# Kernel optimization log

Hardware: AMD Instinct MI355X
Metric: run time of the kernel (lower is better)

Reference implementation:

```python
import jax, jax.numpy as jnp
import numpy as np

B, S, D = 8, 1024, 768
H, DH = 8, 96          # number_of_heads, head_outdim = D // H
DFF = 4 * D            # mlp hidden
EPS = 1e-5


def _p(key, shape, scale=0.02):
    return (jax.random.normal(key, shape, dtype=jnp.float32) * scale)


def setup_inputs() -> dict:
    key = jax.random.key(0)
    ks = jax.random.split(key, 16)
    return {
        "h": jax.random.normal(ks[0], (B, S, D), dtype=jnp.float32),
        "x": jax.random.normal(ks[1], (B, S, D), dtype=jnp.float32),
        # SLN 1: scalar gamma/beta + LayerNorm affine
        "g1": jnp.ones((), jnp.float32), "be1": jnp.zeros((), jnp.float32),
        "ln1_w": jnp.ones((D,), jnp.float32), "ln1_b": jnp.zeros((D,), jnp.float32),
        # SLN 2
        "g2": jnp.ones((), jnp.float32), "be2": jnp.zeros((), jnp.float32),
        "ln2_w": jnp.ones((D,), jnp.float32), "ln2_b": jnp.zeros((D,), jnp.float32),
        # MSA projections (stored as [in, out] for x @ W)
        "Wq": _p(ks[2], (D, H * DH)), "bq": jnp.zeros((H * DH,), jnp.float32),
        "Wk": _p(ks[3], (D, H * DH)), "bk": jnp.zeros((H * DH,), jnp.float32),
        "Wv": _p(ks[4], (D, H * DH)), "bv": jnp.zeros((H * DH,), jnp.float32),
        "Wo": _p(ks[5], (H * DH, D)), "bo": jnp.zeros((D,), jnp.float32),
        # MLP: D -> 4D -> D, relu
        "W1": _p(ks[6], (D, DFF)), "b1": jnp.zeros((DFF,), jnp.float32),
        "W2": _p(ks[7], (DFF, D)), "b2": jnp.zeros((D,), jnp.float32),
    }


def _sln(h, x, gamma, beta, w, b):
    # SLN(h, x) = gamma * x * LayerNorm(h) + beta * x
    mu = jnp.mean(h, axis=-1, keepdims=True)
    var = jnp.var(h, axis=-1, keepdims=True)
    ln = (h - mu) * jax.lax.rsqrt(var + EPS) * w + b
    return gamma * x * ln + beta * x


def _l2_msa(h, Wq, bq, Wk, bk, Wv, bv, Wo, bo):
    # L2-distance multi-head self-attention (lp=2)
    def heads(W, bias):
        y = h @ W + bias                      # [B,S,H*DH]
        return y.reshape(B, S, H, DH).transpose(0, 2, 1, 3)  # [B,H,S,DH]
    q, k, v = heads(Wq, bq), heads(Wk, bk), heads(Wv, bv)
    # pairwise L2 distances via the quadratic expansion (avoids [B,H,S,S,DH])
    q2 = jnp.sum(q * q, axis=-1)              # [B,H,S]
    k2 = jnp.sum(k * k, axis=-1)              # [B,H,S]
    qk = jnp.einsum("bhsd,bhtd->bhst", q, k)  # [B,H,S,S]
    d2 = jnp.maximum(q2[..., :, None] + k2[..., None, :] - 2.0 * qk, 0.0)
    dist = jnp.sqrt(d2)                       # cdist(q, k, p=2)
    attn = jax.nn.softmax(-dist / np.sqrt(DH), axis=-1)
    out = jnp.einsum("bhst,bhtd->bhsd", attn, v)  # [B,H,S,DH]
    out = out.transpose(0, 2, 1, 3).reshape(B, S, H * DH)
    return out @ Wo + bo


def reference(h, x, g1, be1, ln1_w, ln1_b, g2, be2, ln2_w, ln2_b,
              Wq, bq, Wk, bk, Wv, bv, Wo, bo, W1, b1, W2, b2):
    h1 = _sln(h, x, g1, be1, ln1_w, ln1_b)
    htmp = _l2_msa(h1, Wq, bq, Wk, bk, Wv, bv, Wo, bo) + h   # dropout_rate=0 -> identity
    h2 = _sln(htmp, x, g2, be2, ln2_w, ln2_b)
    hf = jax.nn.relu(h2 @ W1 + b1) @ W2 + b2 + htmp
    return (x, hf)
```

## Files before the change

kernel.cpp:

```cpp
#include <hip/hip_runtime.h>
#include <math.h>

#define B_ 8
#define S_ 1024
#define D_ 768
#define H_ 8
#define DH_ 96
#define DFF_ 3072
#define NTOK (B_*S_)
#define QKVW 2304
#define EPS_ 1e-5f

typedef __attribute__((ext_vector_type(4))) float f4;
typedef __attribute__((ext_vector_type(4))) int i4;
typedef __attribute__((ext_vector_type(8))) __bf16 bf16x8;
typedef __attribute__((ext_vector_type(4))) unsigned short us4;
typedef __attribute__((ext_vector_type(8))) unsigned short us8;

static __device__ __forceinline__ unsigned short f2bf(float f) {
    unsigned int u = __builtin_bit_cast(unsigned int, f);
    u += 0x7fffu + ((u >> 16) & 1u);
    return (unsigned short)(u >> 16);
}
static __device__ __forceinline__ float bf2f(unsigned short u) {
    unsigned int x = ((unsigned int)u) << 16;
    return __builtin_bit_cast(float, x);
}

#define GLOBAL_LOAD_LDS16(g, l) \
    __builtin_amdgcn_global_load_lds((const __attribute__((address_space(1))) unsigned int*)(g), \
                                     (__attribute__((address_space(3))) unsigned int*)(l), 16, 0, 0)

__global__ __launch_bounds__(192) void sln_kernel(
    const float* __restrict__ h, const float* __restrict__ x,
    const float* __restrict__ gamma, const float* __restrict__ beta,
    const float* __restrict__ w, const float* __restrict__ bvec,
    unsigned short* __restrict__ out_bf, float* __restrict__ xcopy)
{
    int row = blockIdx.x;
    int t = threadIdx.x;
    const float4* h4 = (const float4*)(h + (size_t)row * D_);
    const float4* x4 = (const float4*)(x + (size_t)row * D_);
    float4 hv = h4[t];
    float s  = hv.x + hv.y + hv.z + hv.w;
    float ss = hv.x*hv.x + hv.y*hv.y + hv.z*hv.z + hv.w*hv.w;
    #pragma unroll
    for (int off = 32; off > 0; off >>= 1) {
        s  += __shfl_down(s, off);
        ss += __shfl_down(ss, off);
    }
    __shared__ float red[2][3];
    int wid = t >> 6;
    if ((t & 63) == 0) { red[0][wid] = s; red[1][wid] = ss; }
    __syncthreads();
    float sum   = red[0][0] + red[0][1] + red[0][2];
    float sumsq = red[1][0] + red[1][1] + red[1][2];
    float mu  = sum * (1.0f / D_);
    float var = sumsq * (1.0f / D_) - mu * mu;
    float rstd = rsqrtf(var + EPS_);
    float g = gamma[0], be = beta[0];
    float4 wv = ((const float4*)w)[t];
    float4 bv = ((const float4*)bvec)[t];
    float4 xv = x4[t];
    us4 o;
    o.x = f2bf(xv.x * (g * ((hv.x - mu) * rstd * wv.x + bv.x) + be));
    o.y = f2bf(xv.y * (g * ((hv.y - mu) * rstd * wv.y + bv.y) + be));
    o.z = f2bf(xv.z * (g * ((hv.z - mu) * rstd * wv.z + bv.z) + be));
    o.w = f2bf(xv.w * (g * ((hv.w - mu) * rstd * wv.w + bv.w) + be));
    *(us4*)(out_bf + (size_t)row * D_ + t * 4) = o;
    if (xcopy) ((float4*)(xcopy + (size_t)row * D_))[t] = xv;
}

__global__ __launch_bounds__(256) void prep_all_kernel(
    const float* __restrict__ Wq, const float* __restrict__ Wk,
    const float* __restrict__ Wv, const float* __restrict__ Wo,
    const float* __restrict__ W1, const float* __restrict__ W2,
    const float* __restrict__ bq, const float* __restrict__ bk, const float* __restrict__ bv,
    unsigned short* __restrict__ Wqkvt, unsigned short* __restrict__ Wot,
    unsigned short* __restrict__ W1t, unsigned short* __restrict__ W2t,
    float* __restrict__ bqkv)
{
    int id = blockIdx.x;
    int tx = threadIdx.x, ty = threadIdx.y;
    if (id >= 6912) {
        int i = (id - 6912) * 256 + ty * 32 + tx;
        if (i < QKVW) {
            float v = (i < 768) ? bq[i] : (i < 1536) ? bk[i - 768] : bv[i - 1536];
            bqkv[i] = v;
        }
        return;
    }
    const float* in; unsigned short* out; int K, N, nbx, rel;
    if (id < 1728)      { int m = id / 576; rel = id % 576;
                          in = (m == 0) ? Wq : (m == 1) ? Wk : Wv;
                          out = Wqkvt + (size_t)m * 768 * 768; K = 768; N = 768; nbx = 24; }
    else if (id < 2304) { rel = id - 1728; in = Wo; out = Wot;  K = 768;  N = 768;  nbx = 24; }
    else if (id < 4608) { rel = id - 2304; in = W1; out = W1t;  K = 768;  N = 3072; nbx = 96; }
    else                { rel = id - 4608; in = W2; out = W2t;  K = 3072; N = 768;  nbx = 24; }
    int n0 = (rel % nbx) * 32, k0 = (rel / nbx) * 32;
    __shared__ float tile[32][33];
    #pragma unroll
    for (int r = 0; r < 4; r++)
        tile[ty + r * 8][tx] = in[(size_t)(k0 + ty + r * 8) * N + n0 + tx];
    __syncthreads();
    #pragma unroll
    for (int r = 0; r < 4; r++)
        out[(size_t)(n0 + ty + r * 8) * K + k0 + tx] = f2bf(tile[tx][ty + r * 8]);
}

template<int OUT_BF16, int RELU>
__global__ __launch_bounds__(256) void gemm_mfma_kernel(
    const unsigned short* __restrict__ A, const unsigned short* __restrict__ Bt,
    const float* __restrict__ bias, const float* __restrict__ resid,
    void* __restrict__ Cout, int M, int N, int K)
{
    __shared__ unsigned short Asm[2][128 * 32];
    __shared__ unsigned short Bsm[2][128 * 32];

    int t = threadIdx.x;
    int lane = t & 63, wv = t >> 6;
    int wm = wv & 1, wn = wv >> 1;
    int l16 = lane & 15, quad = lane >> 4;

    int bm = blockIdx.x * 128;
    int bn = blockIdx.y * 128;

    const unsigned short* Abase = A  + (size_t)bm * K;
    const unsigned short* Bbase = Bt + (size_t)bn * K;

    int fl0 = t, fl1 = 256 + t;
    int r0 = fl0 >> 2, lg0 = (fl0 ^ (fl0 >> 3)) & 3;
    int r1 = fl1 >> 2, lg1 = (fl1 ^ (fl1 >> 3)) & 3;

    f4 acc[4][4] = {};

    GLOBAL_LOAD_LDS16(Abase + (size_t)r0 * K + lg0 * 8, &Asm[0][fl0 * 8]);
    GLOBAL_LOAD_LDS16(Abase + (size_t)r1 * K + lg1 * 8, &Asm[0][fl1 * 8]);
    GLOBAL_LOAD_LDS16(Bbase + (size_t)r0 * K + lg0 * 8, &Bsm[0][fl0 * 8]);
    GLOBAL_LOAD_LDS16(Bbase + (size_t)r1 * K + lg1 * 8, &Bsm[0][fl1 * 8]);
    __syncthreads();

    int nk = K >> 5;
    int cur = 0;
    for (int it = 0; it < nk; ++it) {
        if (it + 1 < nk) {
            int k0 = (it + 1) << 5;
            GLOBAL_LOAD_LDS16(Abase + (size_t)r0 * K + k0 + lg0 * 8, &Asm[cur ^ 1][fl0 * 8]);
            GLOBAL_LOAD_LDS16(Abase + (size_t)r1 * K + k0 + lg1 * 8, &Asm[cur ^ 1][fl1 * 8]);
            GLOBAL_LOAD_LDS16(Bbase + (size_t)r0 * K + k0 + lg0 * 8, &Bsm[cur ^ 1][fl0 * 8]);
            GLOBAL_LOAD_LDS16(Bbase + (size_t)r1 * K + k0 + lg1 * 8, &Bsm[cur ^ 1][fl1 * 8]);
        }

        bf16x8 xf[4], wf[4];
        #pragma unroll
        for (int i = 0; i < 4; i++) {
            int m = wm * 64 + i * 16 + l16;
            int p = (quad ^ (m >> 1)) & 3;
            xf[i] = __builtin_bit_cast(bf16x8, *(const i4*)&Asm[cur][m * 32 + p * 8]);
        }
        #pragma unroll
        for (int j = 0; j < 4; j++) {
            int n = wn * 64 + j * 16 + l16;
            int p = (quad ^ (n >> 1)) & 3;
            wf[j] = __builtin_bit_cast(bf16x8, *(const i4*)&Bsm[cur][n * 32 + p * 8]);
        }
        #pragma unroll
        for (int j = 0; j < 4; j++)
            #pragma unroll
            for (int i = 0; i < 4; i++)
                acc[j][i] = __builtin_amdgcn_mfma_f32_16x16x32_bf16(wf[j], xf[i], acc[j][i], 0, 0, 0);

        __syncthreads();
        cur ^= 1;
    }

    #pragma unroll
    for (int i = 0; i < 4; i++) {
        int rowg = bm + wm * 64 + i * 16 + l16;
        #pragma unroll
        for (int j = 0; j < 4; j++) {
            int colg0 = bn + wn * 64 + j * 16 + quad * 4;
            f4 v = acc[j][i];
            f4 b4 = *(const f4*)&bias[colg0];
            v += b4;
            if (RELU) {
                #pragma unroll
                for (int r = 0; r < 4; r++) v[r] = fmaxf(v[r], 0.f);
            }
            if (resid) {
                f4 r4 = *(const f4*)&resid[(size_t)rowg * N + colg0];
                v += r4;
            }
            if (OUT_BF16) {
                us4 o;
                o.x = f2bf(v[0]); o.y = f2bf(v[1]); o.z = f2bf(v[2]); o.w = f2bf(v[3]);
                *(us4*)((unsigned short*)Cout + (size_t)rowg * N + colg0) = o;
            } else {
                *(f4*)((float*)Cout + (size_t)rowg * N + colg0) = v;
            }
        }
    }
}

template<int OUT_BF16, int RELU>
__global__ __launch_bounds__(256) void gemm_mfma_n64_kernel(
    const unsigned short* __restrict__ A, const unsigned short* __restrict__ Bt,
    const float* __restrict__ bias, const float* __restrict__ resid,
    void* __restrict__ Cout, int M, int N, int K)
{
    __shared__ unsigned short Asm[2][128 * 64];
    __shared__ unsigned short Bsm[2][64 * 64];

    int t = threadIdx.x;
    int lane = t & 63, wv = t >> 6;
    int wm = wv & 1, wn = wv >> 1;
    int l16 = lane & 15, quad = lane >> 4;

    int bm = blockIdx.x * 128;
    int bn = blockIdx.y * 64;

    const unsigned short* Abase = A  + (size_t)bm * K;
    const unsigned short* Bbase = Bt + (size_t)bn * K;

    int ar[4], alg[4], br[2], blg[2];
    #pragma unroll
    for (int i = 0; i < 4; i++) {
        int fl = t + i * 256;
        ar[i] = fl >> 3; alg[i] = (fl ^ (fl >> 3)) & 7;
    }
    #pragma unroll
    for (int i = 0; i < 2; i++) {
        int fl = t + i * 256;
        br[i] = fl >> 3; blg[i] = (fl ^ (fl >> 3)) & 7;
    }

    f4 acc[2][4] = {};

    #pragma unroll
    for (int i = 0; i < 4; i++)
        GLOBAL_LOAD_LDS16(Abase + (size_t)ar[i] * K + alg[i] * 8, &Asm[0][(t + i * 256) * 8]);
    #pragma unroll
    for (int i = 0; i < 2; i++)
        GLOBAL_LOAD_LDS16(Bbase + (size_t)br[i] * K + blg[i] * 8, &Bsm[0][(t + i * 256) * 8]);
    __syncthreads();

    int nk = K >> 6;
    int cur = 0;
    for (int it = 0; it < nk; ++it) {
        if (it + 1 < nk) {
            int k0 = (it + 1) << 6;
            #pragma unroll
            for (int i = 0; i < 4; i++)
                GLOBAL_LOAD_LDS16(Abase + (size_t)ar[i] * K + k0 + alg[i] * 8, &Asm[cur ^ 1][(t + i * 256) * 8]);
            #pragma unroll
            for (int i = 0; i < 2; i++)
                GLOBAL_LOAD_LDS16(Bbase + (size_t)br[i] * K + k0 + blg[i] * 8, &Bsm[cur ^ 1][(t + i * 256) * 8]);
        }

        #pragma unroll
        for (int kk = 0; kk < 2; kk++) {
            bf16x8 xf[4], wf[2];
            #pragma unroll
            for (int i = 0; i < 4; i++) {
                int m = wm * 64 + i * 16 + l16;
                int p = ((kk * 4 + quad) ^ (m & 7)) & 7;
                xf[i] = __builtin_bit_cast(bf16x8, *(const i4*)&Asm[cur][m * 64 + p * 8]);
            }
            #pragma unroll
            for (int j = 0; j < 2; j++) {
                int n = wn * 32 + j * 16 + l16;
                int p = ((kk * 4 + quad) ^ (n & 7)) & 7;
                wf[j] = __builtin_bit_cast(bf16x8, *(const i4*)&Bsm[cur][n * 64 + p * 8]);
            }
            #pragma unroll
            for (int j = 0; j < 2; j++)
                #pragma unroll
                for (int i = 0; i < 4; i++)
                    acc[j][i] = __builtin_amdgcn_mfma_f32_16x16x32_bf16(wf[j], xf[i], acc[j][i], 0, 0, 0);
        }

        __syncthreads();
        cur ^= 1;
    }

    #pragma unroll
    for (int i = 0; i < 4; i++) {
        int rowg = bm + wm * 64 + i * 16 + l16;
        #pragma unroll
        for (int j = 0; j < 2; j++) {
            int colg0 = bn + wn * 32 + j * 16 + quad * 4;
            f4 v = acc[j][i];
            f4 b4 = *(const f4*)&bias[colg0];
            v += b4;
            if (RELU) {
                #pragma unroll
                for (int r = 0; r < 4; r++) v[r] = fmaxf(v[r], 0.f);
            }
            if (resid) {
                f4 r4 = *(const f4*)&resid[(size_t)rowg * N + colg0];
                v += r4;
            }
            if (OUT_BF16) {
                us4 o;
                o.x = f2bf(v[0]); o.y = f2bf(v[1]); o.z = f2bf(v[2]); o.w = f2bf(v[3]);
                *(us4*)((unsigned short*)Cout + (size_t)rowg * N + colg0) = o;
            } else {
                *(f4*)((float*)Cout + (size_t)rowg * N + colg0) = v;
            }
        }
    }
}

__global__ __launch_bounds__(256) void norms_kernel(
    const unsigned short* __restrict__ qkv, float* __restrict__ q2g, float* __restrict__ k2g)
{
    int row = blockIdx.x;
    int t = threadIdx.x;
    int hh = t >> 5, l32 = t & 31;
    const unsigned short* base = qkv + (size_t)row * QKVW + hh * DH_ + l32 * 3;
    float qs = 0.f, ks = 0.f;
    #pragma unroll
    for (int e = 0; e < 3; e++) {
        float qv = bf2f(base[e]);
        float kv = bf2f(base[768 + e]);
        qs += qv * qv; ks += kv * kv;
    }
    #pragma unroll
    for (int off = 16; off > 0; off >>= 1) {
        qs += __shfl_xor(qs, off, 32);
        ks += __shfl_xor(ks, off, 32);
    }
    if (l32 == 0) {
        int b = row >> 10, s = row & 1023;
        int idx = (b * H_ + hh) * S_ + s;
        q2g[idx] = qs; k2g[idx] = ks;
    }
}

__global__ __launch_bounds__(256) void vtrans_kernel(
    const unsigned short* __restrict__ qkv, unsigned short* __restrict__ vt)
{
    __shared__ unsigned short Vl[64][100];
    int blk = blockIdx.x;
    int bh = blk >> 4, kt = blk & 15;
    int b = bh >> 3, hh = bh & 7;
    int t = threadIdx.x;
    int key = t >> 2, qc = t & 3;
    const unsigned short* src = qkv + ((size_t)(b * S_ + kt * 64 + key)) * QKVW + 1536 + hh * DH_;
    #pragma unroll
    for (int i = 0; i < 3; i++) {
        int chunk = qc + i * 4;
        us8 v = *(const us8*)(src + chunk * 8);
        #pragma unroll
        for (int e = 0; e < 8; e++) Vl[key][chunk * 8 + e] = v[e];
    }
    __syncthreads();
    unsigned short* dst = vt + (size_t)blk * 7168;
    #pragma unroll
    for (int r = 0; r < 3; r++) {
        int c = r * 256 + t;
        int vd = c >> 3, kc = c & 7;
        us8 o;
        #pragma unroll
        for (int j = 0; j < 8; j++) o[j] = Vl[kc * 8 + j][vd];
        *(us8*)(dst + vd * 72 + kc * 8) = o;
    }
}

__global__ __launch_bounds__(256, 4) void attn_mfma_kernel(
    const unsigned short* __restrict__ qkv,
    const unsigned short* __restrict__ vt,
    const float* __restrict__ q2g, const float* __restrict__ k2g,
    unsigned short* __restrict__ outb)
{
    __shared__ unsigned short Klds[64 * 96];
    __shared__ unsigned short Vlds[7168];
    __shared__ unsigned short Plds[4][16 * 72];

    int t = threadIdx.x;
    int lane = t & 63, w = t >> 6;
    int l16 = lane & 15, quad = lane >> 4;

    int bh = blockIdx.x >> 4;
    int qt = blockIdx.x & 15;
    int b = bh >> 3, hh = bh & 7;

    int qrow0 = qt * 64 + w * 16;

    const unsigned short* qb = qkv + ((size_t)(b * S_ + qrow0)) * QKVW + hh * DH_;
    bf16x8 qf[3];
    #pragma unroll
    for (int d = 0; d < 3; d++)
        qf[d] = __builtin_bit_cast(bf16x8,
            *(const i4*)(qb + (size_t)l16 * QKVW + d * 32 + quad * 8));

    float q2n = q2g[bh * S_ + qrow0 + l16];

    float lsum = 0.f;
    f4 Oacc[6] = {};

    const float cexp = 0.14724445f;

    const unsigned short* kgb = qkv + ((size_t)(b * S_)) * QKVW + 768 + hh * DH_;
    const unsigned short* vgb0 = vt + (size_t)(bh * 16) * 7168;

    for (int it = 0; it < 16; it++) {
        __syncthreads();
        #pragma unroll
        for (int r = 0; r < 3; r++) {
            int c = r * 256 + t;
            int key = c / 12, dc = c % 12;
            GLOBAL_LOAD_LDS16(kgb + ((size_t)(it * 64 + key)) * QKVW + dc * 8, &Klds[c * 8]);
        }
        const unsigned short* vgb = vgb0 + (size_t)it * 7168;
        #pragma unroll
        for (int r = 0; r < 3; r++)
            GLOBAL_LOAD_LDS16(vgb + (r * 256 + t) * 8, &Vlds[(r * 256 + t) * 8]);
        if (t < 128)
            GLOBAL_LOAD_LDS16(vgb + (768 + t) * 8, &Vlds[(768 + t) * 8]);
        __syncthreads();

        #pragma unroll
        for (int kt2 = 0; kt2 < 4; kt2++) {
            bf16x8 kf0 = __builtin_bit_cast(bf16x8, *(const i4*)&Klds[(kt2 * 16 + l16) * 96 + quad * 8]);
            bf16x8 kf1 = __builtin_bit_cast(bf16x8, *(const i4*)&Klds[(kt2 * 16 + l16) * 96 + 32 + quad * 8]);
            bf16x8 kf2 = __builtin_bit_cast(bf16x8, *(const i4*)&Klds[(kt2 * 16 + l16) * 96 + 64 + quad * 8]);
            f4 a = {};
            a = __builtin_amdgcn_mfma_f32_16x16x32_bf16(kf0, qf[0], a, 0, 0, 0);
            a = __builtin_amdgcn_mfma_f32_16x16x32_bf16(kf1, qf[1], a, 0, 0, 0);
            a = __builtin_amdgcn_mfma_f32_16x16x32_bf16(kf2, qf[2], a, 0, 0, 0);
            float4 k2f = *(const float4*)(k2g + bh * S_ + it * 64 + kt2 * 16 + quad * 4);
            float pk2[4] = {k2f.x + q2n, k2f.y + q2n, k2f.z + q2n, k2f.w + q2n};
            #pragma unroll
            for (int r2 = 0; r2 < 4; r2++) {
                float d2 = fmaxf(pk2[r2] - 2.f * a[r2], 0.f);
                float p = exp2f(-__builtin_amdgcn_sqrtf(d2) * cexp);
                lsum += p;
                a[r2] = p;
            }
            uint2 pkd;
            pkd.x = (unsigned)f2bf(a[0]) | ((unsigned)f2bf(a[1]) << 16);
            pkd.y = (unsigned)f2bf(a[2]) | ((unsigned)f2bf(a[3]) << 16);
            *(uint2*)&Plds[w][l16 * 72 + kt2 * 16 + quad * 4] = pkd;
        }
        bf16x8 pa0 = __builtin_bit_cast(bf16x8, *(const i4*)&Plds[w][l16 * 72 + quad * 8]);
        bf16x8 pa1 = __builtin_bit_cast(bf16x8, *(const i4*)&Plds[w][l16 * 72 + 32 + quad * 8]);
        #pragma unroll
        for (int vtl = 0; vtl < 6; vtl++) {
            bf16x8 vf0 = __builtin_bit_cast(bf16x8, *(const i4*)&Vlds[(vtl * 16 + l16) * 72 + quad * 8]);
            bf16x8 vf1 = __builtin_bit_cast(bf16x8, *(const i4*)&Vlds[(vtl * 16 + l16) * 72 + 32 + quad * 8]);
            Oacc[vtl] = __builtin_amdgcn_mfma_f32_16x16x32_bf16(pa0, vf0, Oacc[vtl], 0, 0, 0);
            Oacc[vtl] = __builtin_amdgcn_mfma_f32_16x16x32_bf16(pa1, vf1, Oacc[vtl], 0, 0, 0);
        }
    }
    lsum += __shfl_xor(lsum, 16, 64);
    lsum += __shfl_xor(lsum, 32, 64);
    float inv_l = 1.f / lsum;
    f4 iv;
    #pragma unroll
    for (int r2 = 0; r2 < 4; r2++)
        iv[r2] = __shfl(inv_l, quad * 4 + r2, 64);
    #pragma unroll
    for (int vtl = 0; vtl < 6; vtl++)
        #pragma unroll
        for (int r2 = 0; r2 < 4; r2++) {
            int row = b * S_ + qrow0 + quad * 4 + r2;
            outb[(size_t)row * D_ + hh * DH_ + vtl * 16 + l16] = f2bf(Oacc[vtl][r2] * iv[r2]);
        }
}

extern "C" void kernel_launch(void* const* d_in, const int* in_sizes, int n_in,
                              void* d_out, int out_size, void* d_ws, size_t ws_size,
                              hipStream_t stream)
{
    const float* h    = (const float*)d_in[0];
    const float* x    = (const float*)d_in[1];
    const float* g1   = (const float*)d_in[2];
    const float* be1  = (const float*)d_in[3];
    const float* ln1w = (const float*)d_in[4];
    const float* ln1b = (const float*)d_in[5];
    const float* g2   = (const float*)d_in[6];
    const float* be2  = (const float*)d_in[7];
    const float* ln2w = (const float*)d_in[8];
    const float* ln2b = (const float*)d_in[9];
    const float* Wq   = (const float*)d_in[10];
    const float* bq   = (const float*)d_in[11];
    const float* Wk   = (const float*)d_in[12];
    const float* bk   = (const float*)d_in[13];
    const float* Wv   = (const float*)d_in[14];
    const float* bv   = (const float*)d_in[15];
    const float* Wo   = (const float*)d_in[16];
    const float* bo   = (const float*)d_in[17];
    const float* W1   = (const float*)d_in[18];
    const float* b1   = (const float*)d_in[19];
    const float* W2   = (const float*)d_in[20];
    const float* b2   = (const float*)d_in[21];

    float* out = (float*)d_out;
    char* wsb = (char*)d_ws;
    const size_t ND = (size_t)NTOK * D_;

    size_t off = 0;
    unsigned short* W1t = (unsigned short*)(wsb + off); off += 4718592;
    unsigned short* W2t = (unsigned short*)(wsb + off); off += 4718592;
    float* bqkv = (float*)(wsb + off);                  off += 16384;
    float* htmp = (float*)(wsb + off);                  off += ND * 4;
    float* q2g  = (float*)(wsb + off);                  off += (size_t)B_ * H_ * S_ * 4;
    float* k2g  = (float*)(wsb + off);                  off += (size_t)B_ * H_ * S_ * 4;
    unsigned short* h2b = (unsigned short*)(wsb + off); off += ND * 2;
    size_t pool0 = off;
    unsigned short* Wqkvt = (unsigned short*)(wsb + off); off += 3538944;
    unsigned short* Wot   = (unsigned short*)(wsb + off); off += 1179648;
    unsigned short* h1b   = (unsigned short*)(wsb + off); off += ND * 2;
    unsigned short* vtg   = (unsigned short*)(wsb + off); off += (size_t)1024 * 14336;
    unsigned short* qkvb  = (unsigned short*)(wsb + off); off += (size_t)NTOK * QKVW * 2;
    unsigned short* attnb   = h1b;
    unsigned short* hiddenb = (unsigned short*)(wsb + pool0);

    prep_all_kernel<<<6921, dim3(32, 8), 0, stream>>>(
        Wq, Wk, Wv, Wo, W1, W2, bq, bk, bv, Wqkvt, Wot, W1t, W2t, bqkv);

    sln_kernel<<<NTOK, 192, 0, stream>>>(h, x, g1, be1, ln1w, ln1b, h1b, out);

    gemm_mfma_kernel<1, 0><<<dim3(NTOK/128, QKVW/128), 256, 0, stream>>>(
        h1b, Wqkvt, bqkv, nullptr, qkvb, NTOK, QKVW, D_);

    norms_kernel<<<NTOK, 256, 0, stream>>>(qkvb, q2g, k2g);
    vtrans_kernel<<<1024, 256, 0, stream>>>(qkvb, vtg);

    attn_mfma_kernel<<<1024, 256, 0, stream>>>(qkvb, vtg, q2g, k2g, attnb);

    gemm_mfma_n64_kernel<0, 0><<<dim3(NTOK/128, D_/64), 256, 0, stream>>>(
        attnb, Wot, bo, h, htmp, NTOK, D_, D_);

    sln_kernel<<<NTOK, 192, 0, stream>>>(htmp, x, g2, be2, ln2w, ln2b, h2b, nullptr);

    gemm_mfma_kernel<1, 1><<<dim3(NTOK/128, DFF_/128), 256, 0, stream>>>(
        h2b, W1t, b1, nullptr, hiddenb, NTOK, DFF_, D_);
    gemm_mfma_n64_kernel<0, 0><<<dim3(NTOK/128, D_/64), 256, 0, stream>>>(
        hiddenb, W2t, b2, htmp, out + ND, NTOK, D_, DFF_);

    (void)in_sizes; (void)n_in; (void)out_size; (void)ws_size;
}
```

Measured before the change: 424.2 us.

## Fold -2 scale into K weights, relayout K tile, remap attention blocks

Pre-scales the K projection weights and bias by -2 and stores k2 as 0.25*|k|^2, so the MFMA accumulator starts at q2+k2 and yields d2 directly. This removes the per-element subtract and multiply. The K tile in LDS is relaid out dim-chunk-major to cut LDS bank conflicts. k2 loads are hoisted ahead of the barrier, bf16 packing uses the hardware v_cvt_pk_bf16_f32 instruction, and block-to-(batch,head) mapping is interleaved. Risks: scaling K by -2 in bf16 is exact, and the asm conversion may round differently from the manual routine.

```diff
diff --git a/kernel.cpp b/kernel.cpp
--- a/kernel.cpp
+++ b/kernel.cpp
@@ -85,14 +85,16 @@
     if (id >= 6912) {
         int i = (id - 6912) * 256 + ty * 32 + tx;
         if (i < QKVW) {
-            float v = (i < 768) ? bq[i] : (i < 1536) ? bk[i - 768] : bv[i - 1536];
+            float v = (i < 768) ? bq[i] : (i < 1536) ? -2.f * bk[i - 768] : bv[i - 1536];
             bqkv[i] = v;
         }
         return;
     }
     const float* in; unsigned short* out; int K, N, nbx, rel;
+    float scl = 1.f;
     if (id < 1728)      { int m = id / 576; rel = id % 576;
                           in = (m == 0) ? Wq : (m == 1) ? Wk : Wv;
+                          if (m == 1) scl = -2.f;
                           out = Wqkvt + (size_t)m * 768 * 768; K = 768; N = 768; nbx = 24; }
     else if (id < 2304) { rel = id - 1728; in = Wo; out = Wot;  K = 768;  N = 768;  nbx = 24; }
     else if (id < 4608) { rel = id - 2304; in = W1; out = W1t;  K = 768;  N = 3072; nbx = 96; }
@@ -105,7 +107,7 @@
     __syncthreads();
     #pragma unroll
     for (int r = 0; r < 4; r++)
-        out[(size_t)(n0 + ty + r * 8) * K + k0 + tx] = f2bf(tile[tx][ty + r * 8]);
+        out[(size_t)(n0 + ty + r * 8) * K + k0 + tx] = f2bf(scl * tile[tx][ty + r * 8]);
 }
 
 template<int OUT_BF16, int RELU>
@@ -333,7 +335,7 @@
     if (l32 == 0) {
         int b = row >> 10, s = row & 1023;
         int idx = (b * H_ + hh) * S_ + s;
-        q2g[idx] = qs; k2g[idx] = ks;
+        q2g[idx] = qs; k2g[idx] = ks * 0.25f;
     }
 }
 
@@ -381,8 +383,10 @@
     int lane = t & 63, w = t >> 6;
     int l16 = lane & 15, quad = lane >> 4;
 
-    int bh = blockIdx.x >> 4;
-    int qt = blockIdx.x & 15;
+    int bid = blockIdx.x;
+    int slot = bid >> 3;
+    int bh = (bid & 7) * 8 + (slot >> 4);
+    int qt = slot & 15;
     int b = bh >> 3, hh = bh & 7;
 
     int qrow0 = qt * 64 + w * 16;
@@ -403,13 +407,19 @@
 
     const unsigned short* kgb = qkv + ((size_t)(b * S_)) * QKVW + 768 + hh * DH_;
     const unsigned short* vgb0 = vt + (size_t)(bh * 16) * 7168;
+    const float* k2base = k2g + bh * S_;
 
     for (int it = 0; it < 16; it++) {
+        float4 k2f[4];
+        #pragma unroll
+        for (int kt2 = 0; kt2 < 4; kt2++)
+            k2f[kt2] = *(const float4*)(k2base + it * 64 + kt2 * 16 + quad * 4);
+
         __syncthreads();
         #pragma unroll
         for (int r = 0; r < 3; r++) {
             int c = r * 256 + t;
-            int key = c / 12, dc = c % 12;
+            int key = c & 63, dc = c >> 6;
             GLOBAL_LOAD_LDS16(kgb + ((size_t)(it * 64 + key)) * QKVW + dc * 8, &Klds[c * 8]);
         }
         const unsigned short* vgb = vgb0 + (size_t)it * 7168;
@@ -420,27 +430,28 @@
             GLOBAL_LOAD_LDS16(vgb + (768 + t) * 8, &Vlds[(768 + t) * 8]);
         __syncthreads();
 
+        const unsigned short* kB = &Klds[quad * 512 + l16 * 8];
         #pragma unroll
         for (int kt2 = 0; kt2 < 4; kt2++) {
-            bf16x8 kf0 = __builtin_bit_cast(bf16x8, *(const i4*)&Klds[(kt2 * 16 + l16) * 96 + quad * 8]);
-            bf16x8 kf1 = __builtin_bit_cast(bf16x8, *(const i4*)&Klds[(kt2 * 16 + l16) * 96 + 32 + quad * 8]);
-            bf16x8 kf2 = __builtin_bit_cast(bf16x8, *(const i4*)&Klds[(kt2 * 16 + l16) * 96 + 64 + quad * 8]);
-            f4 a = {};
+            const unsigned short* kp = kB + kt2 * 128;
+            bf16x8 kf0 = __builtin_bit_cast(bf16x8, *(const i4*)(kp));
+            bf16x8 kf1 = __builtin_bit_cast(bf16x8, *(const i4*)(kp + 2048));
+            bf16x8 kf2 = __builtin_bit_cast(bf16x8, *(const i4*)(kp + 4096));
+            f4 a = {k2f[kt2].x + q2n, k2f[kt2].y + q2n, k2f[kt2].z + q2n, k2f[kt2].w + q2n};
             a = __builtin_amdgcn_mfma_f32_16x16x32_bf16(kf0, qf[0], a, 0, 0, 0);
             a = __builtin_amdgcn_mfma_f32_16x16x32_bf16(kf1, qf[1], a, 0, 0, 0);
             a = __builtin_amdgcn_mfma_f32_16x16x32_bf16(kf2, qf[2], a, 0, 0, 0);
-            float4 k2f = *(const float4*)(k2g + bh * S_ + it * 64 + kt2 * 16 + quad * 4);
-            float pk2[4] = {k2f.x + q2n, k2f.y + q2n, k2f.z + q2n, k2f.w + q2n};
             #pragma unroll
             for (int r2 = 0; r2 < 4; r2++) {
-                float d2 = fmaxf(pk2[r2] - 2.f * a[r2], 0.f);
+                float d2 = fmaxf(a[r2], 0.f);
                 float p = exp2f(-__builtin_amdgcn_sqrtf(d2) * cexp);
                 lsum += p;
                 a[r2] = p;
             }
-            uint2 pkd;
-            pkd.x = (unsigned)f2bf(a[0]) | ((unsigned)f2bf(a[1]) << 16);
-            pkd.y = (unsigned)f2bf(a[2]) | ((unsigned)f2bf(a[3]) << 16);
+            unsigned int plo, phi;
+            asm("v_cvt_pk_bf16_f32 %0, %1, %2" : "=v"(plo) : "v"(a[0]), "v"(a[1]));
+            asm("v_cvt_pk_bf16_f32 %0, %1, %2" : "=v"(phi) : "v"(a[2]), "v"(a[3]));
+            uint2 pkd; pkd.x = plo; pkd.y = phi;
             *(uint2*)&Plds[w][l16 * 72 + kt2 * 16 + quad * 4] = pkd;
         }
         bf16x8 pa0 = __builtin_bit_cast(bf16x8, *(const i4*)&Plds[w][l16 * 72 + quad * 8]);
```

Result: no change. 429.3 us (+1.2%).
